# Kernel tuning notes

Hardware: AMD Instinct MI355X
Metric: run time of the kernel (lower is better)

## Reference

```python
import jax, jax.numpy as jnp
import numpy as np

N_NODES = 100000

def sage_conv(x, edge_index, Wl, bl, Wr):
    # PyG SAGEConv, aggr='add', normalize=False:
    #   out = lin_l(sum_{j in N(i)} x_j) + lin_r(x_i)
    src, dst = edge_index[0], edge_index[1]
    agg = jax.ops.segment_sum(x[src], dst, num_segments=N_NODES)  # [N, F]
    return agg @ Wl.T + bl + x @ Wr.T


def setup_inputs() -> dict:
    key = jax.random.key(0)
    ks = jax.random.split(key, 7)
    F_IN, HID, C, E = 128, 256, 50, 640000
    x = jax.random.normal(ks[0], (N_NODES, F_IN), dtype=jnp.float32)
    edge_index = jax.random.randint(ks[1], (2, E), 0, N_NODES, dtype=jnp.int64)
    s1 = 1.0 / np.sqrt(F_IN)
    s2 = 1.0 / np.sqrt(HID)
    return {
        "x": x,
        "edge_index": edge_index,
        "W1l": jax.random.normal(ks[2], (HID, F_IN), dtype=jnp.float32) * s1,
        "b1l": jnp.zeros((HID,), dtype=jnp.float32),
        "W1r": jax.random.normal(ks[3], (HID, F_IN), dtype=jnp.float32) * s1,
        "W2l": jax.random.normal(ks[4], (C, HID), dtype=jnp.float32) * s2,
        "b2l": jnp.zeros((C,), dtype=jnp.float32),
        "W2r": jax.random.normal(ks[5], (C, HID), dtype=jnp.float32) * s2,
    }


def reference(x, edge_index, W1l, b1l, W1r, W2l, b2l, W2r):
    h = sage_conv(x, edge_index, W1l, b1l, W1r)
    h = jax.nn.relu(h)
    # F.dropout(p=0.5, training=False) is identity in eval mode
    out = sage_conv(h, edge_index, W2l, b2l, W2r)
    return out
```

## Files before the change

### kernel.cpp

```cpp
#include <hip/hip_runtime.h>

#define N_NODES 100000
#define MPAD    100096
#define F_IN 128
#define HID 256
#define C_OUT 50
#define N_EDGES 640000
#define CAP 32
#define NXCD 8
#define NODES_PER_XCD 12500
#define NSLICES 256
#define EPS (N_EDGES / NSLICES)
#define SBLK (NSLICES * NXCD)
#define XBLK 12500

typedef __attribute__((ext_vector_type(8))) short short8;
typedef __attribute__((ext_vector_type(8))) ushort us8;
typedef __attribute__((ext_vector_type(4))) float f32x4;

struct alignas(8) us4 { ushort x, y, z, w; };

__device__ __forceinline__ ushort f2bf(float f) {
    union { float f; unsigned u; } v; v.f = f;
    unsigned r = (v.u + 0x7fffu + ((v.u >> 16) & 1u)) >> 16;
    return (ushort)r;
}

__device__ __forceinline__ float bf2f(ushort u) {
    union { unsigned u; float f; } v; v.u = ((unsigned)u) << 16;
    return v.f;
}

__device__ __forceinline__ void load_lds16(const void* gsrc, void* lds) {
    __builtin_amdgcn_global_load_lds(
        (const __attribute__((address_space(1))) void*)gsrc,
        (__attribute__((address_space(3))) void*)lds, 16, 0, 0);
}

__global__ void prep_kernel(const float* __restrict__ W1l, const float* __restrict__ W1r,
                            const float* __restrict__ W2l, const float* __restrict__ W2r,
                            ushort* __restrict__ B1t, ushort* __restrict__ B2t,
                            int* __restrict__ cnt) {
    int idx = blockIdx.x * blockDim.x + threadIdx.x;
    if (idx < N_NODES) cnt[idx] = 0;
    if (idx < 256 * 256) {
        int o = idx >> 8, k = idx & 255;
        float v = (k < 128) ? W1l[o * 128 + k] : W1r[o * 128 + (k - 128)];
        B1t[o * 256 + k] = f2bf(v);
    }
    if (idx < 128 * 256) {
        int c = idx >> 8, k = idx & 255;
        float v = 0.f;
        if (c < C_OUT) v = W2l[c * 256 + k];
        else if (c >= 64 && c < 64 + C_OUT) v = W2r[(c - 64) * 256 + k];
        B2t[c * 256 + k] = f2bf(v);
    }
}

__global__ __launch_bounds__(256) void scatter_xcvt(const int* __restrict__ src,
                                                    const int* __restrict__ dst,
                                                    int* __restrict__ cnt,
                                                    int* __restrict__ bucket,
                                                    const float* __restrict__ x,
                                                    ushort* __restrict__ A1) {
    int b = blockIdx.x;
    if (b < SBLK) {
        int xcd = b & (NXCD - 1);
        int slice = b >> 3;
        int lo = xcd * NODES_PER_XCD;
        int hi = lo + NODES_PER_XCD;
        int base = slice * EPS;
        for (int i = base + (int)threadIdx.x; i < base + EPS; i += 256) {
            int d = dst[i];
            int s = src[i];
            if (d >= lo && d < hi) {
                int p = atomicAdd(&cnt[d], 1);
                if (p < CAP) bucket[(size_t)d * CAP + p] = s;
            }
        }
    } else {
        int tid = (b - SBLK) * 256 + threadIdx.x;
        int node = tid >> 5, q = tid & 31;
        if (node >= N_NODES) return;
        float4 v = *reinterpret_cast<const float4*>(x + (size_t)node * F_IN + q * 4);
        us4 o;
        o.x = f2bf(v.x); o.y = f2bf(v.y); o.z = f2bf(v.z); o.w = f2bf(v.w);
        *reinterpret_cast<us4*>(&A1[(size_t)node * 256 + 128 + q * 4]) = o;
    }
}

__global__ void gather1_kernel(const int* __restrict__ cnt, const int* __restrict__ bucket,
                               ushort* __restrict__ A1) {
    int tid = blockIdx.x * blockDim.x + threadIdx.x;
    int node = tid >> 4, q = tid & 15;
    if (node >= N_NODES) return;
    int n = cnt[node];
    if (n > CAP) n = CAP;
    const int* row = bucket + (size_t)node * CAP;
    float a[8];
#pragma unroll
    for (int j = 0; j < 8; ++j) a[j] = 0.f;
    int p = 0;
    while (p + 8 <= n) {
        us8 v[8];
#pragma unroll
        for (int t = 0; t < 8; ++t) {
            int s = row[p + t];
            v[t] = *reinterpret_cast<const us8*>(&A1[(size_t)s * 256 + 128 + q * 8]);
        }
#pragma unroll
        for (int t = 0; t < 8; ++t)
#pragma unroll
            for (int j = 0; j < 8; ++j) a[j] += bf2f(v[t][j]);
        p += 8;
    }
    int rem = n - p;
    if (rem > 0) {
        us8 v[7];
#pragma unroll
        for (int t = 0; t < 7; ++t) {
            int s = (t < rem) ? row[p + t] : row[p];
            v[t] = *reinterpret_cast<const us8*>(&A1[(size_t)s * 256 + 128 + q * 8]);
        }
#pragma unroll
        for (int t = 0; t < 7; ++t) {
            if (t < rem) {
#pragma unroll
                for (int j = 0; j < 8; ++j) a[j] += bf2f(v[t][j]);
            }
        }
    }
    us8 o;
#pragma unroll
    for (int j = 0; j < 8; ++j) o[j] = f2bf(a[j]);
    *reinterpret_cast<us8*>(&A1[(size_t)node * 256 + q * 8]) = o;
}

__global__ void gather2_kernel(const ushort* __restrict__ g, const int* __restrict__ cnt,
                               const int* __restrict__ bucket, float* __restrict__ out) {
    int tid = blockIdx.x * blockDim.x + threadIdx.x;
    int node = tid >> 3, q = tid & 7;
    if (node >= N_NODES) return;
    int c = q * 8;
    if (c >= C_OUT) return;
    int n = cnt[node];
    if (n > CAP) n = CAP;
    const int* row = bucket + (size_t)node * CAP;
    float a[8];
#pragma unroll
    for (int j = 0; j < 8; ++j) a[j] = 0.f;
    int p = 0;
    while (p + 8 <= n) {
        us8 v[8];
#pragma unroll
        for (int t = 0; t < 8; ++t) {
            int s = row[p + t];
            v[t] = *reinterpret_cast<const us8*>(&g[(size_t)s * 64 + c]);
        }
#pragma unroll
        for (int t = 0; t < 8; ++t)
#pragma unroll
            for (int j = 0; j < 8; ++j) a[j] += bf2f(v[t][j]);
        p += 8;
    }
    int rem = n - p;
    if (rem > 0) {
        us8 v[7];
#pragma unroll
        for (int t = 0; t < 7; ++t) {
            int s = (t < rem) ? row[p + t] : row[p];
            v[t] = *reinterpret_cast<const us8*>(&g[(size_t)s * 64 + c]);
        }
#pragma unroll
        for (int t = 0; t < 7; ++t) {
            if (t < rem) {
#pragma unroll
                for (int j = 0; j < 8; ++j) a[j] += bf2f(v[t][j]);
            }
        }
    }
    float* po = out + (size_t)node * C_OUT;
#pragma unroll
    for (int j = 0; j < 8; ++j) {
        if (c + j < C_OUT) po[c + j] += a[j];
    }
}

__global__ __launch_bounds__(512) void gemm1_512(
    const ushort* __restrict__ A, const ushort* __restrict__ B,
    const float* __restrict__ bias, ushort* __restrict__ hOut) {
    __shared__ alignas(16) ushort As[128 * 32];
    __shared__ alignas(16) ushort Bs[256 * 32];
    const int tid = threadIdx.x;
    const int lane = tid & 63, wid = tid >> 6;
    const int wr = wid >> 2, wc = wid & 3;
    const int brow = blockIdx.x;

    f32x4 acc[4][4];
#pragma unroll
    for (int m = 0; m < 4; ++m)
#pragma unroll
        for (int n = 0; n < 4; ++n) acc[m][n] = (f32x4){0.f, 0.f, 0.f, 0.f};

    const int rA = tid >> 2,          kA = (tid & 3) * 8;
    const int cB1 = tid + 512;
    const int rB0 = tid >> 2,         kB0 = (tid & 3) * 8;
    const int rB1 = cB1 >> 2,         kB1 = (cB1 & 3) * 8;
    const size_t aRow = (size_t)(brow * 128 + rA) * 256;
    const size_t bRow0 = (size_t)rB0 * 256;
    const size_t bRow1 = (size_t)rB1 * 256;

    const int aoffA = (lane & 15) * 32 + (lane >> 4) * 8;

    for (int kt = 0; kt < 8; ++kt) {
        const int kOff = kt * 32;
        load_lds16(A + aRow + kOff + kA, &As[tid * 8]);
        load_lds16(B + bRow0 + kOff + kB0, &Bs[tid * 8]);
        load_lds16(B + bRow1 + kOff + kB1, &Bs[cB1 * 8]);
        __syncthreads();

        short8 af[4], bfr[4];
#pragma unroll
        for (int m = 0; m < 4; ++m)
            af[m] = *reinterpret_cast<const short8*>(&As[(wr * 64 + m * 16) * 32 + aoffA]);
#pragma unroll
        for (int n = 0; n < 4; ++n)
            bfr[n] = *reinterpret_cast<const short8*>(&Bs[(wc * 64 + n * 16) * 32 + aoffA]);
#pragma unroll
        for (int m = 0; m < 4; ++m)
#pragma unroll
            for (int n = 0; n < 4; ++n)
                acc[m][n] = __builtin_amdgcn_mfma_f32_16x16x32_bf16(af[m], bfr[n], acc[m][n], 0, 0, 0);
        __syncthreads();
    }

    const int colB = wc * 64 + (lane & 15);
    const int rowB = brow * 128 + wr * 64 + ((lane >> 4) << 2);

    float bv[4];
#pragma unroll
    for (int n = 0; n < 4; ++n) bv[n] = bias[colB + n * 16];
#pragma unroll
    for (int m = 0; m < 4; ++m) {
#pragma unroll
        for (int r = 0; r < 4; ++r) {
            int row = rowB + m * 16 + r;
            if (row >= N_NODES) continue;
#pragma unroll
            for (int n = 0; n < 4; ++n) {
                float v = acc[m][n][r] + bv[n];
                v = v > 0.f ? v : 0.f;
                hOut[(size_t)row * 256 + colB + n * 16] = f2bf(v);
            }
        }
    }
}

__global__ __launch_bounds__(256) void gemm2_kernel(
    const ushort* __restrict__ A, const ushort* __restrict__ B,
    const float* __restrict__ bias, ushort* __restrict__ gOut,
    float* __restrict__ oOut) {
    __shared__ alignas(16) ushort As[128 * 32];
    __shared__ alignas(16) ushort Bs[128 * 32];
    const int tid = threadIdx.x;
    const int lane = tid & 63, wid = tid >> 6;
    const int wr = wid >> 1, wc = wid & 1;
    const int brow = blockIdx.x;

    f32x4 acc[4][4];
#pragma unroll
    for (int m = 0; m < 4; ++m)
#pragma unroll
        for (int n = 0; n < 4; ++n) acc[m][n] = (f32x4){0.f, 0.f, 0.f, 0.f};

    const int c0 = tid, c1 = tid + 256;
    const int r0 = c0 >> 2, k80 = (c0 & 3) * 8;
    const int r1 = c1 >> 2, k81 = (c1 & 3) * 8;
    const size_t aRow0 = (size_t)(brow * 128 + r0) * 256;
    const size_t aRow1 = (size_t)(brow * 128 + r1) * 256;
    const size_t bRow0 = (size_t)r0 * 256;
    const size_t bRow1 = (size_t)r1 * 256;

    const int aoffA = (lane & 15) * 32 + (lane >> 4) * 8;

    for (int kt = 0; kt < 8; ++kt) {
        const int kOff = kt * 32;
        load_lds16(A + aRow0 + kOff + k80, &As[c0 * 8]);
        load_lds16(A + aRow1 + kOff + k81, &As[c1 * 8]);
        load_lds16(B + bRow0 + kOff + k80, &Bs[c0 * 8]);
        load_lds16(B + bRow1 + kOff + k81, &Bs[c1 * 8]);
        __syncthreads();

        short8 af[4], bfr[4];
#pragma unroll
        for (int m = 0; m < 4; ++m)
            af[m] = *reinterpret_cast<const short8*>(&As[(wr * 64 + m * 16) * 32 + aoffA]);
#pragma unroll
        for (int n = 0; n < 4; ++n)
            bfr[n] = *reinterpret_cast<const short8*>(&Bs[(wc * 64 + n * 16) * 32 + aoffA]);
#pragma unroll
        for (int m = 0; m < 4; ++m)
#pragma unroll
            for (int n = 0; n < 4; ++n)
                acc[m][n] = __builtin_amdgcn_mfma_f32_16x16x32_bf16(af[m], bfr[n], acc[m][n], 0, 0, 0);
        __syncthreads();
    }

    const int colB = wc * 64 + (lane & 15);
    const int rowB = brow * 128 + wr * 64 + ((lane >> 4) << 2);

#pragma unroll
    for (int m = 0; m < 4; ++m) {
#pragma unroll
        for (int r = 0; r < 4; ++r) {
            int row = rowB + m * 16 + r;
            if (row >= N_NODES) continue;
#pragma unroll
            for (int n = 0; n < 4; ++n) {
                int cg = colB + n * 16;
                float v = acc[m][n][r];
                if (cg < 64) {
                    gOut[(size_t)row * 64 + cg] = f2bf(v);
                } else if (cg < 64 + C_OUT) {
                    oOut[(size_t)row * C_OUT + (cg - 64)] = v + bias[cg - 64];
                }
            }
        }
    }
}

extern "C" void kernel_launch(void* const* d_in, const int* in_sizes, int n_in,
                              void* d_out, int out_size, void* d_ws, size_t ws_size,
                              hipStream_t stream) {
    const float* x   = (const float*)d_in[0];
    const int*   ei  = (const int*)d_in[1];
    const float* W1l = (const float*)d_in[2];
    const float* b1l = (const float*)d_in[3];
    const float* W1r = (const float*)d_in[4];
    const float* W2l = (const float*)d_in[5];
    const float* b2l = (const float*)d_in[6];
    const float* W2r = (const float*)d_in[7];
    float* out = (float*)d_out;

    ushort* A1   = (ushort*)d_ws;
    ushort* hbuf = A1 + (size_t)MPAD * 256;
    ushort* B1t  = hbuf + (size_t)MPAD * 256;
    ushort* B2t  = B1t + 256 * 256;
    ushort* g    = B2t + 128 * 256;
    int* cnt     = (int*)(g + (size_t)N_NODES * 64);
    int* bucket  = cnt + N_NODES;

    const int* src = ei;
    const int* dst = ei + N_EDGES;

    prep_kernel<<<391, 256, 0, stream>>>(W1l, W1r, W2l, W2r, B1t, B2t, cnt);
    scatter_xcvt<<<SBLK + XBLK, 256, 0, stream>>>(src, dst, cnt, bucket, x, A1);

    gather1_kernel<<<(N_NODES * 16 + 255) / 256, 256, 0, stream>>>(cnt, bucket, A1);

    const int nbrow = MPAD / 128;
    gemm1_512<<<nbrow, 512, 0, stream>>>(A1, B1t, b1l, hbuf);
    gemm2_kernel<<<nbrow, 256, 0, stream>>>(hbuf, B2t, b2l, g, out);

    gather2_kernel<<<(N_NODES * 8 + 255) / 256, 256, 0, stream>>>(g, cnt, bucket, out);
}
```

Baseline: 162.7 us.

## Replace global-atomic CSR build with two-phase LDS bucketing and fuse both GEMMs

The edge bucketing now runs in two phases. First, per-block LDS counters bin edges into 256-node ranges. Then a per-range merge kernel builds the per-node buckets in shared memory and writes them out coalesced. This replaces the global atomics and the 8x redundant edge scans of the old XCD-sliced scatter. Separately, the two GEMMs are fused: the ReLU'd hidden tile is kept in LDS and fed directly into the second GEMM, which removes the hbuf round trip through HBM and one launch. The costs are an extra merge launch, heavy LDS use (72KB) that may limit occupancy, and a per-block cap of 32 edges per range that could silently drop edges under skew.

Result: no change. 165.8 us (+1.9%).

```diff
diff --git a/kernel.cpp b/kernel.cpp
--- a/kernel.cpp
+++ b/kernel.cpp
@@ -7,11 +7,10 @@
 #define C_OUT 50
 #define N_EDGES 640000
 #define CAP 32
-#define NXCD 8
-#define NODES_PER_XCD 12500
-#define NSLICES 256
-#define EPS (N_EDGES / NSLICES)
-#define SBLK (NSLICES * NXCD)
+#define NRANGE 391
+#define P1BLK 256
+#define EPB (N_EDGES / P1BLK)
+#define CCAP 32
 #define XBLK 12500
 
 typedef __attribute__((ext_vector_type(8))) short short8;
@@ -39,10 +38,8 @@
 
 __global__ void prep_kernel(const float* __restrict__ W1l, const float* __restrict__ W1r,
                             const float* __restrict__ W2l, const float* __restrict__ W2r,
-                            ushort* __restrict__ B1t, ushort* __restrict__ B2t,
-                            int* __restrict__ cnt) {
+                            ushort* __restrict__ B1t, ushort* __restrict__ B2t) {
     int idx = blockIdx.x * blockDim.x + threadIdx.x;
-    if (idx < N_NODES) cnt[idx] = 0;
     if (idx < 256 * 256) {
         int o = idx >> 8, k = idx & 255;
         float v = (k < 128) ? W1l[o * 128 + k] : W1r[o * 128 + (k - 128)];
@@ -57,35 +54,61 @@
     }
 }
 
-__global__ __launch_bounds__(256) void scatter_xcvt(const int* __restrict__ src,
-                                                    const int* __restrict__ dst,
-                                                    int* __restrict__ cnt,
-                                                    int* __restrict__ bucket,
-                                                    const float* __restrict__ x,
-                                                    ushort* __restrict__ A1) {
+__global__ __launch_bounds__(256) void phase1_xcvt(const int* __restrict__ src,
+                                                   const int* __restrict__ dst,
+                                                   int* __restrict__ cnt1,
+                                                   int* __restrict__ subbucket,
+                                                   const float* __restrict__ x,
+                                                   ushort* __restrict__ A1) {
+    __shared__ int lcnt[NRANGE];
     int b = blockIdx.x;
-    if (b < SBLK) {
-        int xcd = b & (NXCD - 1);
-        int slice = b >> 3;
-        int lo = xcd * NODES_PER_XCD;
-        int hi = lo + NODES_PER_XCD;
-        int base = slice * EPS;
-        for (int i = base + (int)threadIdx.x; i < base + EPS; i += 256) {
+    if (b < P1BLK) {
+        for (int r = threadIdx.x; r < NRANGE; r += 256) lcnt[r] = 0;
+        __syncthreads();
+        int base = b * EPB;
+        for (int i = base + (int)threadIdx.x; i < base + EPB; i += 256) {
             int d = dst[i];
             int s = src[i];
-            if (d >= lo && d < hi) {
-                int p = atomicAdd(&cnt[d], 1);
-                if (p < CAP) bucket[(size_t)d * CAP + p] = s;
-            }
-        }
+            int r = d >> 8;
+            int p = atomicAdd(&lcnt[r], 1);
+            if (p < CCAP) subbucket[((size_t)r * P1BLK + b) * CCAP + p] = ((d & 255) << 24) | s;
+        }
+        __syncthreads();
+        for (int r = threadIdx.x; r < NRANGE; r += 256) cnt1[r * P1BLK + b] = lcnt[r];
     } else {
-        int tid = (b - SBLK) * 256 + threadIdx.x;
+        int tid = (b - P1BLK) * 256 + threadIdx.x;
         int node = tid >> 5, q = tid & 31;
         if (node >= N_NODES) return;
         float4 v = *reinterpret_cast<const float4*>(x + (size_t)node * F_IN + q * 4);
         us4 o;
         o.x = f2bf(v.x); o.y = f2bf(v.y); o.z = f2bf(v.z); o.w = f2bf(v.w);
         *reinterpret_cast<us4*>(&A1[(size_t)node * 256 + 128 + q * 4]) = o;
+    }
+}
+
+__global__ __launch_bounds__(256) void phase2_merge(const int* __restrict__ cnt1,
+                                                    const int* __restrict__ subbucket,
+                                                    int* __restrict__ cnt,
+                                                    int* __restrict__ bucket) {
+    __shared__ int lcnt2[256];
+    __shared__ int lbuf[256 * CAP];
+    int r = blockIdx.x, t = threadIdx.x;
+    lcnt2[t] = 0;
+    __syncthreads();
+    int n = cnt1[r * P1BLK + t];
+    if (n > CCAP) n = CCAP;
+    size_t cbase = ((size_t)r * P1BLK + t) * CCAP;
+    for (int k = 0; k < n; ++k) {
+        unsigned u = (unsigned)subbucket[cbase + k];
+        int dl = u >> 24;
+        int p = atomicAdd(&lcnt2[dl], 1);
+        if (p < CAP) lbuf[dl * CAP + p] = (int)(u & 0xFFFFFF);
+    }
+    __syncthreads();
+    int node0 = r << 8;
+    if (node0 + t < N_NODES) cnt[node0 + t] = lcnt2[t];
+    for (int idx = t; idx < 256 * CAP; idx += 256) {
+        if (node0 + (idx >> 5) < N_NODES) bucket[(size_t)node0 * CAP + idx] = lbuf[idx];
     }
 }
 
@@ -186,15 +209,22 @@
     }
 }
 
-__global__ __launch_bounds__(512) void gemm1_512(
-    const ushort* __restrict__ A, const ushort* __restrict__ B,
-    const float* __restrict__ bias, ushort* __restrict__ hOut) {
-    __shared__ alignas(16) ushort As[128 * 32];
-    __shared__ alignas(16) ushort Bs[256 * 32];
+__global__ __launch_bounds__(512) void gemm_fused(
+    const ushort* __restrict__ A, const ushort* __restrict__ B1,
+    const ushort* __restrict__ B2, const float* __restrict__ b1,
+    const float* __restrict__ b2, ushort* __restrict__ gOut,
+    float* __restrict__ oOut) {
+    __shared__ alignas(16) ushort smem[36864];
+    ushort* As  = smem;
+    ushort* Bs  = smem + 4096;
+    ushort* hL  = smem;
+    ushort* Bs2 = smem + 32768;
+
     const int tid = threadIdx.x;
     const int lane = tid & 63, wid = tid >> 6;
     const int wr = wid >> 2, wc = wid & 3;
     const int brow = blockIdx.x;
+    const int aoffA = (lane & 15) * 32 + (lane >> 4) * 8;
 
     f32x4 acc[4][4];
 #pragma unroll
@@ -202,21 +232,16 @@
 #pragma unroll
         for (int n = 0; n < 4; ++n) acc[m][n] = (f32x4){0.f, 0.f, 0.f, 0.f};
 
-    const int rA = tid >> 2,          kA = (tid & 3) * 8;
+    const int rA = tid >> 2, kA = (tid & 3) * 8;
     const int cB1 = tid + 512;
-    const int rB0 = tid >> 2,         kB0 = (tid & 3) * 8;
-    const int rB1 = cB1 >> 2,         kB1 = (cB1 & 3) * 8;
+    const int rB1 = cB1 >> 2, kB1 = (cB1 & 3) * 8;
     const size_t aRow = (size_t)(brow * 128 + rA) * 256;
-    const size_t bRow0 = (size_t)rB0 * 256;
-    const size_t bRow1 = (size_t)rB1 * 256;
-
-    const int aoffA = (lane & 15) * 32 + (lane >> 4) * 8;
 
     for (int kt = 0; kt < 8; ++kt) {
         const int kOff = kt * 32;
         load_lds16(A + aRow + kOff + kA, &As[tid * 8]);
-        load_lds16(B + bRow0 + kOff + kB0, &Bs[tid * 8]);
-        load_lds16(B + bRow1 + kOff + kB1, &Bs[cB1 * 8]);
+        load_lds16(B1 + (size_t)rA * 256 + kOff + kA, &Bs[tid * 8]);
+        load_lds16(B1 + (size_t)rB1 * 256 + kOff + kB1, &Bs[cB1 * 8]);
         __syncthreads();
 
         short8 af[4], bfr[4];
@@ -234,12 +259,58 @@
         __syncthreads();
     }
 
-    const int colB = wc * 64 + (lane & 15);
+    {
+        const int colBase = wc * 64 + (lane & 15);
+        const int lrBase = wr * 64 + ((lane >> 4) << 2);
+        float bv[4];
+#pragma unroll
+        for (int n = 0; n < 4; ++n) bv[n] = b1[colBase + n * 16];
+#pragma unroll
+        for (int m = 0; m < 4; ++m) {
+#pragma unroll
+            for (int r = 0; r < 4; ++r) {
+                int lr = lrBase + m * 16 + r;
+#pragma unroll
+                for (int n = 0; n < 4; ++n) {
+                    float v = acc[m][n][r] + bv[n];
+                    v = v > 0.f ? v : 0.f;
+                    int ktc = wc * 2 + (n >> 1);
+                    int kp = (n & 1) * 16 + (lane & 15);
+                    hL[ktc * 4096 + lr * 32 + kp] = f2bf(v);
+                }
+            }
+        }
+    }
+    __syncthreads();
+
+    f32x4 acc2[4][2];
+#pragma unroll
+    for (int m = 0; m < 4; ++m)
+#pragma unroll
+        for (int n = 0; n < 2; ++n) acc2[m][n] = (f32x4){0.f, 0.f, 0.f, 0.f};
+
+    for (int kt = 0; kt < 8; ++kt) {
+        const int kOff = kt * 32;
+        load_lds16(B2 + (size_t)rA * 256 + kOff + kA, &Bs2[tid * 8]);
+        __syncthreads();
+
+        short8 af[4], bfr[2];
+#pragma unroll
+        for (int m = 0; m < 4; ++m)
+            af[m] = *reinterpret_cast<const short8*>(&hL[kt * 4096 + (wr * 64 + m * 16) * 32 + aoffA]);
+#pragma unroll
+        for (int n = 0; n < 2; ++n)
+            bfr[n] = *reinterpret_cast<const short8*>(&Bs2[(wc * 32 + n * 16) * 32 + aoffA]);
+#pragma unroll
+        for (int m = 0; m < 4; ++m)
+#pragma unroll
+            for (int n = 0; n < 2; ++n)
+                acc2[m][n] = __builtin_amdgcn_mfma_f32_16x16x32_bf16(af[m], bfr[n], acc2[m][n], 0, 0, 0);
+        __syncthreads();
+    }
+
+    const int colB = wc * 32 + (lane & 15);
     const int rowB = brow * 128 + wr * 64 + ((lane >> 4) << 2);
-
-    float bv[4];
-#pragma unroll
-    for (int n = 0; n < 4; ++n) bv[n] = bias[colB + n * 16];
 #pragma unroll
     for (int m = 0; m < 4; ++m) {
 #pragma unroll
@@ -247,82 +318,13 @@
             int row = rowB + m * 16 + r;
             if (row >= N_NODES) continue;
 #pragma unroll
-            for (int n = 0; n < 4; ++n) {
-                float v = acc[m][n][r] + bv[n];
-                v = v > 0.f ? v : 0.f;
-                hOut[(size_t)row * 256 + colB + n * 16] = f2bf(v);
-            }
-        }
-    }
-}
-
-__global__ __launch_bounds__(256) void gemm2_kernel(
-    const ushort* __restrict__ A, const ushort* __restrict__ B,
-    const float* __restrict__ bias, ushort* __restrict__ gOut,
-    float* __restrict__ oOut) {
-    __shared__ alignas(16) ushort As[128 * 32];
-    __shared__ alignas(16) ushort Bs[128 * 32];
-    const int tid = threadIdx.x;
-    const int lane = tid & 63, wid = tid >> 6;
-    const int wr = wid >> 1, wc = wid & 1;
-    const int brow = blockIdx.x;
-
-    f32x4 acc[4][4];
-#pragma unroll
-    for (int m = 0; m < 4; ++m)
-#pragma unroll
-        for (int n = 0; n < 4; ++n) acc[m][n] = (f32x4){0.f, 0.f, 0.f, 0.f};
-
-    const int c0 = tid, c1 = tid + 256;
-    const int r0 = c0 >> 2, k80 = (c0 & 3) * 8;
-    const int r1 = c1 >> 2, k81 = (c1 & 3) * 8;
-    const size_t aRow0 = (size_t)(brow * 128 + r0) * 256;
-    const size_t aRow1 = (size_t)(brow * 128 + r1) * 256;
-    const size_t bRow0 = (size_t)r0 * 256;
-    const size_t bRow1 = (size_t)r1 * 256;
-
-    const int aoffA = (lane & 15) * 32 + (lane >> 4) * 8;
-
-    for (int kt = 0; kt < 8; ++kt) {
-        const int kOff = kt * 32;
-        load_lds16(A + aRow0 + kOff + k80, &As[c0 * 8]);
-        load_lds16(A + aRow1 + kOff + k81, &As[c1 * 8]);
-        load_lds16(B + bRow0 + kOff + k80, &Bs[c0 * 8]);
-        load_lds16(B + bRow1 + kOff + k81, &Bs[c1 * 8]);
-        __syncthreads();
-
-        short8 af[4], bfr[4];
-#pragma unroll
-        for (int m = 0; m < 4; ++m)
-            af[m] = *reinterpret_cast<const short8*>(&As[(wr * 64 + m * 16) * 32 + aoffA]);
-#pragma unroll
-        for (int n = 0; n < 4; ++n)
-            bfr[n] = *reinterpret_cast<const short8*>(&Bs[(wc * 64 + n * 16) * 32 + aoffA]);
-#pragma unroll
-        for (int m = 0; m < 4; ++m)
-#pragma unroll
-            for (int n = 0; n < 4; ++n)
-                acc[m][n] = __builtin_amdgcn_mfma_f32_16x16x32_bf16(af[m], bfr[n], acc[m][n], 0, 0, 0);
-        __syncthreads();
-    }
-
-    const int colB = wc * 64 + (lane & 15);
-    const int rowB = brow * 128 + wr * 64 + ((lane >> 4) << 2);
-
-#pragma unroll
-    for (int m = 0; m < 4; ++m) {
-#pragma unroll
-        for (int r = 0; r < 4; ++r) {
-            int row = rowB + m * 16 + r;
-            if (row >= N_NODES) continue;
-#pragma unroll
-            for (int n = 0; n < 4; ++n) {
+            for (int n = 0; n < 2; ++n) {
                 int cg = colB + n * 16;
-                float v = acc[m][n][r];
+                float v = acc2[m][n][r];
                 if (cg < 64) {
                     gOut[(size_t)row * 64 + cg] = f2bf(v);
                 } else if (cg < 64 + C_OUT) {
-                    oOut[(size_t)row * C_OUT + (cg - 64)] = v + bias[cg - 64];
+                    oOut[(size_t)row * C_OUT + (cg - 64)] = v + b2[cg - 64];
                 }
             }
         }
@@ -342,25 +344,26 @@
     const float* W2r = (const float*)d_in[7];
     float* out = (float*)d_out;
 
-    ushort* A1   = (ushort*)d_ws;
-    ushort* hbuf = A1 + (size_t)MPAD * 256;
-    ushort* B1t  = hbuf + (size_t)MPAD * 256;
-    ushort* B2t  = B1t + 256 * 256;
-    ushort* g    = B2t + 128 * 256;
-    int* cnt     = (int*)(g + (size_t)N_NODES * 64);
-    int* bucket  = cnt + N_NODES;
+    ushort* A1    = (ushort*)d_ws;
+    ushort* B1t   = A1 + (size_t)MPAD * 256;
+    ushort* B2t   = B1t + 256 * 256;
+    ushort* g     = B2t + 128 * 256;
+    int* cnt      = (int*)(g + (size_t)N_NODES * 64);
+    int* bucket   = cnt + N_NODES;
+    int* cnt1     = bucket + (size_t)N_NODES * CAP;
+    int* subbucket= cnt1 + NRANGE * P1BLK;
 
     const int* src = ei;
     const int* dst = ei + N_EDGES;
 
-    prep_kernel<<<391, 256, 0, stream>>>(W1l, W1r, W2l, W2r, B1t, B2t, cnt);
-    scatter_xcvt<<<SBLK + XBLK, 256, 0, stream>>>(src, dst, cnt, bucket, x, A1);
+    prep_kernel<<<256, 256, 0, stream>>>(W1l, W1r, W2l, W2r, B1t, B2t);
+    phase1_xcvt<<<P1BLK + XBLK, 256, 0, stream>>>(src, dst, cnt1, subbucket, x, A1);
+    phase2_merge<<<NRANGE, 256, 0, stream>>>(cnt1, subbucket, cnt, bucket);
 
     gather1_kernel<<<(N_NODES * 16 + 255) / 256, 256, 0, stream>>>(cnt, bucket, A1);
 
     const int nbrow = MPAD / 128;
-    gemm1_512<<<nbrow, 512, 0, stream>>>(A1, B1t, b1l, hbuf);
-    gemm2_kernel<<<nbrow, 256, 0, stream>>>(hbuf, B2t, b2l, g, out);
+    gemm_fused<<<nbrow, 512, 0, stream>>>(A1, B1t, B2t, b1l, b2l, g, out);
 
     gather2_kernel<<<(N_NODES * 8 + 255) / 256, 256, 0, stream>>>(g, cnt, bucket, out);
 }
```
